# Kernel optimization log

Hardware: AMD Instinct MI355X
Metric: run time of the kernel (lower is better)

## Reference

```python
import jax, jax.numpy as jnp
import numpy as np

RADIUS = 5.0          # cutoff radius (Angstrom)
MAX_NBR = 32          # max_num_neighbors_threshold
CELL_L = 12.0         # cubic box edge; > 2*RADIUS/2 so rep=1 (27 image cells)


def setup_inputs() -> dict:
    key = jax.random.key(0)
    k1, _ = jax.random.split(key)
    B, N = 16, 256
    pos = jax.random.uniform(k1, (B, N, 3), dtype=jnp.float32) * CELL_L
    cell = jnp.tile(jnp.eye(3, dtype=jnp.float32)[None] * CELL_L, (B, 1, 1))
    return {"pos": pos, "cell": cell}


def reference(pos, cell):
    # pos: [B,N,3] atom positions, cell: [B,3,3] lattice vectors (rows a1,a2,a3)
    B, N, _ = pos.shape
    # periodic image offsets n in {-1,0,1}^3 -> unit: [C,3], C=27
    r = jnp.arange(-1, 2, dtype=pos.dtype)
    n1, n2, n3 = jnp.meshgrid(r, r, r, indexing="ij")
    unit = jnp.stack([n1.ravel(), n2.ravel(), n3.ravel()], axis=-1)  # [C,3]
    C = unit.shape[0]
    # pbc_offsets[b,c,:] = sum_k n_k * a_k  (== bmm(cell^T, unit^T) in torch code)
    offsets = jnp.einsum("ck,bkd->bcd", unit, cell)  # [B,C,3]
    # candidate edge vectors: receiver i, source j shifted by image offset c
    dvec = pos[:, :, None, None, :] - (pos[:, None, :, None, :] + offsets[:, None, None, :, :])  # [B,N,N,C,3]
    dsqr = jnp.sum(dvec * dvec, axis=-1)  # [B,N,N,C]
    # radius mask + remove self (atom_distance_sqr > 1e-4)
    within = (dsqr <= RADIUS * RADIUS) & (dsqr > 1e-4)
    M = N * C
    dsqr_f = jnp.where(within, dsqr, jnp.inf).reshape(B, N, M)
    # per-receiver sort-based top-K truncation (mirrors get_max_neighbors_mask:
    # index_copy into [num_atoms, max_nbr] padded with inf, sort, keep first K finite)
    order = jnp.argsort(dsqr_f, axis=-1)
    rank = jnp.argsort(order, axis=-1)           # rank of each candidate among its receiver's neighbors
    keep = (rank < MAX_NBR) & jnp.isfinite(dsqr_f)  # [B,N,M] final edge mask
    dist = jnp.where(keep, jnp.sqrt(jnp.where(keep, dsqr_f, 1.0)), 0.0)  # masked edge lengths
    dvec_m = jnp.where(keep[..., None], dvec.reshape(B, N, M, 3), 0.0)   # masked edge vectors
    # num_neighbors_image == segment_csr(clamp(num_neighbors, K)) == per-image kept-edge count
    num_neighbors_image = jnp.sum(keep.reshape(B, -1), axis=-1).astype(jnp.int32)
    return dist, dvec_m, num_neighbors_image
```

## Files before the change

kernel.cpp:

```cpp
#include <hip/hip_runtime.h>
#include <stdint.h>


constexpr int B_ = 16, N_ = 256, C_ = 27;
constexpr int M_ = N_ * C_;
constexpr int MAXC = 256;
constexpr int KMAX = 32;

typedef float vfloat4 __attribute__((ext_vector_type(4)));

__device__ __forceinline__ void nt_store4(float* p, float a, float b, float c, float d) {
    vfloat4 v; v.x = a; v.y = b; v.z = c; v.w = d;
    __builtin_nontemporal_store(v, (vfloat4*)p);
}

__global__ __launch_bounds__(256)
void nbr_kernel(const float* __restrict__ pos,
                const float* __restrict__ cell,
                float* __restrict__ dist,
                float* __restrict__ dvec,
                float* __restrict__ nn)
{
#pragma clang fp contract(off)
    __shared__ float offx[C_], offy[C_], offz[C_];
    __shared__ unsigned long long keys[MAXC];
    __shared__ float4 vals[MAXC];
    __shared__ float4 kept[KMAX];
    __shared__ unsigned char slot[M_];
    __shared__ int cnt;

    const int bi  = blockIdx.x;
    const int b   = bi >> 8;
    const int i   = bi & 255;
    const int tid = threadIdx.x;

    const float* pb = pos + b * N_ * 3;
    const float pjx = pb[tid * 3 + 0], pjy = pb[tid * 3 + 1], pjz = pb[tid * 3 + 2];
    const float pix = pb[i * 3 + 0],   piy = pb[i * 3 + 1],   piz = pb[i * 3 + 2];

    if (tid < C_) {
        const float n1 = (float)(tid / 9 - 1);
        const float n2 = (float)((tid / 3) % 3 - 1);
        const float n3 = (float)(tid % 3 - 1);
        const float* cb = cell + b * 9;
        offx[tid] = n1 * cb[0] + n2 * cb[3] + n3 * cb[6];
        offy[tid] = n1 * cb[1] + n2 * cb[4] + n3 * cb[7];
        offz[tid] = n1 * cb[2] + n2 * cb[5] + n3 * cb[8];
    }
    uint32_t* slot32 = (uint32_t*)slot;
    for (int w = tid; w < M_ / 4; w += 256) slot32[w] = 0;
    if (tid == 0) cnt = 0;
    __syncthreads();

    #pragma unroll 1
    for (int c = 0; c < C_; ++c) {
        const float sx = pjx + offx[c], sy = pjy + offy[c], sz = pjz + offz[c];
        const float dx = pix - sx, dy = piy - sy, dz = piz - sz;
        const float dsq = dx * dx + dy * dy + dz * dz;
        if (dsq <= 25.0f && dsq > 1e-4f) {
            const int idx = atomicAdd(&cnt, 1);
            if (idx < MAXC) {
                keys[idx] = ((unsigned long long)__float_as_uint(dsq) << 32)
                          | (unsigned)(tid * C_ + c);
                vals[idx] = make_float4(dx, dy, dz, dsq);
            }
        }
    }
    __syncthreads();

    int K = cnt; if (K > MAXC) K = MAXC;
    if (tid == 0)
        atomicAdd(&nn[b], (float)(K < KMAX ? K : KMAX));

    for (int idx = tid; idx < K; idx += 256) {
        const unsigned long long key = keys[idx];
        int r = 0;
        for (int q = 0; q < K; ++q) r += (keys[q] < key) ? 1 : 0;
        if (r < KMAX) {
            const int m = (int)(key & 0xffffffffu);
            const float4 v = vals[idx];
            kept[r] = make_float4(v.x, v.y, v.z, sqrtf(v.w));
            slot[m] = (unsigned char)(r + 1);
        }
    }
    __syncthreads();

    float* drow = dist + (size_t)bi * M_;
    float* vrow = dvec + (size_t)bi * (size_t)(M_ * 3);

    {
        float o[4][4];
        #pragma unroll
        for (int k = 0; k < 4; ++k) {
            const int g = tid + k * 256;
            o[k][0] = o[k][1] = o[k][2] = o[k][3] = 0.f;
            const uint32_t s4 = slot32[g];
            if (s4) {
                uint32_t s;
                s = s4 & 0xffu;         if (s) o[k][0] = kept[s - 1].w;
                s = (s4 >> 8) & 0xffu;  if (s) o[k][1] = kept[s - 1].w;
                s = (s4 >> 16) & 0xffu; if (s) o[k][2] = kept[s - 1].w;
                s = (s4 >> 24) & 0xffu; if (s) o[k][3] = kept[s - 1].w;
            }
        }
        #pragma unroll
        for (int k = 0; k < 4; ++k)
            nt_store4(drow + 4 * (tid + k * 256), o[k][0], o[k][1], o[k][2], o[k][3]);
    }
    #pragma unroll
    for (int k = 4; k < 6; ++k) {
        const int g = tid + k * 256;
        float o0 = 0.f, o1 = 0.f, o2 = 0.f, o3 = 0.f;
        const uint32_t s4 = slot32[g];
        if (s4) {
            uint32_t s;
            s = s4 & 0xffu;         if (s) o0 = kept[s - 1].w;
            s = (s4 >> 8) & 0xffu;  if (s) o1 = kept[s - 1].w;
            s = (s4 >> 16) & 0xffu; if (s) o2 = kept[s - 1].w;
            s = (s4 >> 24) & 0xffu; if (s) o3 = kept[s - 1].w;
        }
        nt_store4(drow + 4 * g, o0, o1, o2, o3);
    }
    if (tid < 192) {
        const int g = 1536 + tid;
        float o0 = 0.f, o1 = 0.f, o2 = 0.f, o3 = 0.f;
        const uint32_t s4 = slot32[g];
        if (s4) {
            uint32_t s;
            s = s4 & 0xffu;         if (s) o0 = kept[s - 1].w;
            s = (s4 >> 8) & 0xffu;  if (s) o1 = kept[s - 1].w;
            s = (s4 >> 16) & 0xffu; if (s) o2 = kept[s - 1].w;
            s = (s4 >> 24) & 0xffu; if (s) o3 = kept[s - 1].w;
        }
        nt_store4(drow + 4 * g, o0, o1, o2, o3);
    }

    #pragma unroll 1
    for (int it = 0; it < 5; ++it) {
        const int hbase = it * 1024 + tid;
        float o[4][4];
        #pragma unroll
        for (int k = 0; k < 4; ++k) {
            const int h = hbase + k * 256;
            const int e0 = 4 * h;
            const int m0 = e0 / 3;
            const int m1 = (e0 + 3) / 3;
            o[k][0] = o[k][1] = o[k][2] = o[k][3] = 0.f;
            if ((slot[m0] | slot[m1]) != 0) {
                #pragma unroll
                for (int u = 0; u < 4; ++u) {
                    const int e = e0 + u;
                    const int m = e / 3;
                    const int d = e - 3 * m;
                    const uint32_t s = slot[m];
                    if (s) o[k][u] = (&kept[s - 1].x)[d];
                }
            }
        }
        #pragma unroll
        for (int k = 0; k < 4; ++k)
            nt_store4(vrow + 4 * (hbase + k * 256), o[k][0], o[k][1], o[k][2], o[k][3]);
    }
    if (tid < 64) {
        const int h = 5120 + tid;
        const int e0 = 4 * h;
        const int m0 = e0 / 3;
        const int m1 = (e0 + 3) / 3;
        float o0 = 0.f, o1 = 0.f, o2 = 0.f, o3 = 0.f;
        if ((slot[m0] | slot[m1]) != 0) {
            float oo[4] = {0.f, 0.f, 0.f, 0.f};
            #pragma unroll
            for (int u = 0; u < 4; ++u) {
                const int e = e0 + u;
                const int m = e / 3;
                const int d = e - 3 * m;
                const uint32_t s = slot[m];
                if (s) oo[u] = (&kept[s - 1].x)[d];
            }
            o0 = oo[0]; o1 = oo[1]; o2 = oo[2]; o3 = oo[3];
        }
        nt_store4(vrow + e0, o0, o1, o2, o3);
    }
}

extern "C" void kernel_launch(void* const* d_in, const int* in_sizes, int n_in,
                              void* d_out, int out_size, void* d_ws, size_t ws_size,
                              hipStream_t stream)
{
    const float* pos  = (const float*)d_in[0];
    const float* cell = (const float*)d_in[1];
    float* dist = (float*)d_out;
    float* dvec = dist + (size_t)B_ * N_ * M_;
    float* nn   = dvec + (size_t)B_ * N_ * M_ * 3;
    (void)hipMemsetAsync(nn, 0, B_ * sizeof(float), stream);
    nbr_kernel<<<dim3(B_ * N_), dim3(256), 0, stream>>>(pos, cell, dist, dvec, nn);
}
```

Baseline: 466.6 us.

## Zero-fill outputs up front and scatter only kept edges

Each block now streams zeros over its whole dist and dvec rows with nontemporal vector stores at kernel start, before the neighbor search. After ranking, only the kept edges (at most 32) are scattered into place, using a small kept-index array. This removes the per-candidate byte slot table in LDS and the gather-based output pass. It aims to overlap the dominant output writes with the distance and rank work and to cut LDS use, which may raise occupancy. In exchange it relies on the barrier ordering the zero stores before the later scattered writes, and those scattered writes are narrow and uncoalesced.

```diff
diff --git a/kernel.cpp b/kernel.cpp
--- a/kernel.cpp
+++ b/kernel.cpp
@@ -8,11 +8,6 @@
 constexpr int KMAX = 32;
 
 typedef float vfloat4 __attribute__((ext_vector_type(4)));
-
-__device__ __forceinline__ void nt_store4(float* p, float a, float b, float c, float d) {
-    vfloat4 v; v.x = a; v.y = b; v.z = c; v.w = d;
-    __builtin_nontemporal_store(v, (vfloat4*)p);
-}
 
 __global__ __launch_bounds__(256)
 void nbr_kernel(const float* __restrict__ pos,
@@ -26,7 +21,7 @@
     __shared__ unsigned long long keys[MAXC];
     __shared__ float4 vals[MAXC];
     __shared__ float4 kept[KMAX];
-    __shared__ unsigned char slot[M_];
+    __shared__ int    keptm[KMAX];
     __shared__ int cnt;
 
     const int bi  = blockIdx.x;
@@ -38,6 +33,23 @@
     const float pjx = pb[tid * 3 + 0], pjy = pb[tid * 3 + 1], pjz = pb[tid * 3 + 2];
     const float pix = pb[i * 3 + 0],   piy = pb[i * 3 + 1],   piz = pb[i * 3 + 2];
 
+    float* drow = dist + (size_t)bi * M_;
+    float* vrow = dvec + (size_t)bi * (size_t)(M_ * 3);
+
+    {
+        vfloat4 z; z.x = 0.f; z.y = 0.f; z.z = 0.f; z.w = 0.f;
+        #pragma unroll
+        for (int k = 0; k < 6; ++k)
+            __builtin_nontemporal_store(z, (vfloat4*)(drow + 4 * (tid + k * 256)));
+        if (tid < 192)
+            __builtin_nontemporal_store(z, (vfloat4*)(drow + 4 * (1536 + tid)));
+        #pragma unroll
+        for (int k = 0; k < 20; ++k)
+            __builtin_nontemporal_store(z, (vfloat4*)(vrow + 4 * (tid + k * 256)));
+        if (tid < 64)
+            __builtin_nontemporal_store(z, (vfloat4*)(vrow + 4 * (5120 + tid)));
+    }
+
     if (tid < C_) {
         const float n1 = (float)(tid / 9 - 1);
         const float n2 = (float)((tid / 3) % 3 - 1);
@@ -47,8 +59,6 @@
         offy[tid] = n1 * cb[1] + n2 * cb[4] + n3 * cb[7];
         offz[tid] = n1 * cb[2] + n2 * cb[5] + n3 * cb[8];
     }
-    uint32_t* slot32 = (uint32_t*)slot;
-    for (int w = tid; w < M_ / 4; w += 256) slot32[w] = 0;
     if (tid == 0) cnt = 0;
     __syncthreads();
 
@@ -69,117 +79,31 @@
     __syncthreads();
 
     int K = cnt; if (K > MAXC) K = MAXC;
+    const int nk = K < KMAX ? K : KMAX;
     if (tid == 0)
-        atomicAdd(&nn[b], (float)(K < KMAX ? K : KMAX));
+        atomicAdd(&nn[b], (float)nk);
 
     for (int idx = tid; idx < K; idx += 256) {
         const unsigned long long key = keys[idx];
         int r = 0;
         for (int q = 0; q < K; ++q) r += (keys[q] < key) ? 1 : 0;
         if (r < KMAX) {
-            const int m = (int)(key & 0xffffffffu);
             const float4 v = vals[idx];
-            kept[r] = make_float4(v.x, v.y, v.z, sqrtf(v.w));
-            slot[m] = (unsigned char)(r + 1);
+            kept[r]  = make_float4(v.x, v.y, v.z, sqrtf(v.w));
+            keptm[r] = (int)(key & 0xffffffffu);
         }
     }
+
     __syncthreads();
 
-    float* drow = dist + (size_t)bi * M_;
-    float* vrow = dvec + (size_t)bi * (size_t)(M_ * 3);
-
-    {
-        float o[4][4];
-        #pragma unroll
-        for (int k = 0; k < 4; ++k) {
-            const int g = tid + k * 256;
-            o[k][0] = o[k][1] = o[k][2] = o[k][3] = 0.f;
-            const uint32_t s4 = slot32[g];
-            if (s4) {
-                uint32_t s;
-                s = s4 & 0xffu;         if (s) o[k][0] = kept[s - 1].w;
-                s = (s4 >> 8) & 0xffu;  if (s) o[k][1] = kept[s - 1].w;
-                s = (s4 >> 16) & 0xffu; if (s) o[k][2] = kept[s - 1].w;
-                s = (s4 >> 24) & 0xffu; if (s) o[k][3] = kept[s - 1].w;
-            }
-        }
-        #pragma unroll
-        for (int k = 0; k < 4; ++k)
-            nt_store4(drow + 4 * (tid + k * 256), o[k][0], o[k][1], o[k][2], o[k][3]);
-    }
-    #pragma unroll
-    for (int k = 4; k < 6; ++k) {
-        const int g = tid + k * 256;
-        float o0 = 0.f, o1 = 0.f, o2 = 0.f, o3 = 0.f;
-        const uint32_t s4 = slot32[g];
-        if (s4) {
-            uint32_t s;
-            s = s4 & 0xffu;         if (s) o0 = kept[s - 1].w;
-            s = (s4 >> 8) & 0xffu;  if (s) o1 = kept[s - 1].w;
-            s = (s4 >> 16) & 0xffu; if (s) o2 = kept[s - 1].w;
-            s = (s4 >> 24) & 0xffu; if (s) o3 = kept[s - 1].w;
-        }
-        nt_store4(drow + 4 * g, o0, o1, o2, o3);
-    }
-    if (tid < 192) {
-        const int g = 1536 + tid;
-        float o0 = 0.f, o1 = 0.f, o2 = 0.f, o3 = 0.f;
-        const uint32_t s4 = slot32[g];
-        if (s4) {
-            uint32_t s;
-            s = s4 & 0xffu;         if (s) o0 = kept[s - 1].w;
-            s = (s4 >> 8) & 0xffu;  if (s) o1 = kept[s - 1].w;
-            s = (s4 >> 16) & 0xffu; if (s) o2 = kept[s - 1].w;
-            s = (s4 >> 24) & 0xffu; if (s) o3 = kept[s - 1].w;
-        }
-        nt_store4(drow + 4 * g, o0, o1, o2, o3);
-    }
-
-    #pragma unroll 1
-    for (int it = 0; it < 5; ++it) {
-        const int hbase = it * 1024 + tid;
-        float o[4][4];
-        #pragma unroll
-        for (int k = 0; k < 4; ++k) {
-            const int h = hbase + k * 256;
-            const int e0 = 4 * h;
-            const int m0 = e0 / 3;
-            const int m1 = (e0 + 3) / 3;
-            o[k][0] = o[k][1] = o[k][2] = o[k][3] = 0.f;
-            if ((slot[m0] | slot[m1]) != 0) {
-                #pragma unroll
-                for (int u = 0; u < 4; ++u) {
-                    const int e = e0 + u;
-                    const int m = e / 3;
-                    const int d = e - 3 * m;
-                    const uint32_t s = slot[m];
-                    if (s) o[k][u] = (&kept[s - 1].x)[d];
-                }
-            }
-        }
-        #pragma unroll
-        for (int k = 0; k < 4; ++k)
-            nt_store4(vrow + 4 * (hbase + k * 256), o[k][0], o[k][1], o[k][2], o[k][3]);
-    }
-    if (tid < 64) {
-        const int h = 5120 + tid;
-        const int e0 = 4 * h;
-        const int m0 = e0 / 3;
-        const int m1 = (e0 + 3) / 3;
-        float o0 = 0.f, o1 = 0.f, o2 = 0.f, o3 = 0.f;
-        if ((slot[m0] | slot[m1]) != 0) {
-            float oo[4] = {0.f, 0.f, 0.f, 0.f};
-            #pragma unroll
-            for (int u = 0; u < 4; ++u) {
-                const int e = e0 + u;
-                const int m = e / 3;
-                const int d = e - 3 * m;
-                const uint32_t s = slot[m];
-                if (s) oo[u] = (&kept[s - 1].x)[d];
-            }
-            o0 = oo[0]; o1 = oo[1]; o2 = oo[2]; o3 = oo[3];
-        }
-        nt_store4(vrow + e0, o0, o1, o2, o3);
+    if (tid < nk) {
+        const float4 v = kept[tid];
+        const int m = keptm[tid];
+        drow[m]         = v.w;
+        float* vp = vrow + 3 * m;
+        vp[0] = v.x;
+        vp[1] = v.y;
+        vp[2] = v.z;
     }
 }
 
```

After: 496.6 us. 1.06x slower.
